# Kernel optimization log

Hardware: AMD Instinct MI355X
Metric: run time of the kernel (lower is better)

Reference implementation:

```python
import jax, jax.numpy as jnp
import numpy as np

E, D, MULT, K = 8, 1024, 4, 2   # num_experts, hidden_dim, mlp_multiplier, top-k
B, S = 4, 2048
H = MULT * D


def setup_inputs() -> dict:
    key = jax.random.key(0)
    k0, k1, k2, k3 = jax.random.split(key, 4)
    x = jax.random.normal(k0, (B, S, D), dtype=jnp.float32)
    Wr = jax.random.normal(k1, (E, D), dtype=jnp.float32) * (D ** -0.5)        # router (no bias)
    W1 = jax.random.normal(k2, (E, D, H), dtype=jnp.float32) * (D ** -0.5)     # expert fc1
    b1 = jnp.zeros((E, H), dtype=jnp.float32)
    W2 = jax.random.normal(k3, (E, H, D), dtype=jnp.float32) * (H ** -0.5)     # expert fc2
    b2 = jnp.zeros((E, D), dtype=jnp.float32)
    return {"x": x, "Wr": Wr, "W1": W1, "b1": b1, "W2": W2, "b2": b2}


def reference(x, Wr, W1, b1, W2, b2):
    # Router: softmax over experts then top-k -> per-token combine weights.
    probs = jax.nn.softmax(jnp.einsum("bsd,ed->bse", x, Wr), axis=-1)  # [B,S,E]
    topv, topi = jax.lax.top_k(probs, K)                                # [B,S,K]
    # combine[b,s,e] = sum_k topv * 1[topi==e]  (same math as the masked scatter-add)
    combine = jnp.sum(topv[..., None] * jax.nn.one_hot(topi, E, dtype=x.dtype), axis=2)  # [B,S,E]

    def body(acc, params):
        w1, bb1, w2, bb2, ce = params  # ce: [B,S] combine weight for this expert
        h = jax.nn.gelu(jnp.einsum("bsd,dh->bsh", x, w1) + bb1, approximate=False)
        y = jnp.einsum("bsh,hd->bsd", h, w2) + bb2
        return acc + ce[..., None] * y, None

    cE = jnp.moveaxis(combine, -1, 0)  # [E,B,S]
    out, _ = jax.lax.scan(body, jnp.zeros_like(x), (W1, b1, W2, b2, cE))
    return out
```

## Files before the change

kernel.cpp:

```cpp
#include <hip/hip_runtime.h>
#include <hip/hip_bf16.h>

#define E_   8
#define D_   1024
#define H_   4096
#define T_   8192
#define TMM  128
#define TNN  256
#define BK   64
#define CAP  17408
#define NBY  136
#define CK   2

typedef __attribute__((ext_vector_type(8))) short short8;
typedef __attribute__((ext_vector_type(4))) float floatx4;

__device__ __forceinline__ unsigned short f2bf(float f) {
    unsigned u = __float_as_uint(f);
    u += 0x7fffu + ((u >> 16) & 1u);
    return (unsigned short)(u >> 16);
}
__device__ __forceinline__ float bf2f(unsigned short u) {
    return __uint_as_float((unsigned)u << 16);
}

#define GLP16(g, l)                                                             \
    __builtin_amdgcn_global_load_lds((const __attribute__((address_space(1))) void*)(g), \
                                     (__attribute__((address_space(3))) void*)(l), 16, 0, 0)

__global__ __launch_bounds__(256) void router_kernel(
    const float* __restrict__ x, const float* __restrict__ Wr,
    int* __restrict__ cnt, int* __restrict__ tok_list,
    int2* __restrict__ inv_ei, float2* __restrict__ inv_w)
{
    int t = blockIdx.x * 4 + (threadIdx.x >> 6);
    int lane = threadIdx.x & 63;
    const float4* xr = (const float4*)(x + (size_t)t * D_);
    float acc[E_];
#pragma unroll
    for (int e = 0; e < E_; ++e) acc[e] = 0.f;
#pragma unroll
    for (int it = 0; it < D_ / 256; ++it) {
        float4 xv = xr[lane + it * 64];
#pragma unroll
        for (int e = 0; e < E_; ++e) {
            float4 wv = ((const float4*)(Wr + e * D_))[lane + it * 64];
            acc[e] += xv.x * wv.x + xv.y * wv.y + xv.z * wv.z + xv.w * wv.w;
        }
    }
#pragma unroll
    for (int e = 0; e < E_; ++e) {
#pragma unroll
        for (int off = 32; off; off >>= 1) acc[e] += __shfl_xor(acc[e], off);
    }
    if (lane == 0) {
        float m = acc[0];
#pragma unroll
        for (int e = 1; e < E_; ++e) m = fmaxf(m, acc[e]);
        float p[E_]; float s = 0.f;
#pragma unroll
        for (int e = 0; e < E_; ++e) { p[e] = expf(acc[e] - m); s += p[e]; }
        float inv = 1.f / s;
        int i1 = 0; float v1 = p[0];
#pragma unroll
        for (int e = 1; e < E_; ++e) if (p[e] > v1) { v1 = p[e]; i1 = e; }
        int i2 = -1; float v2 = -1.f;
#pragma unroll
        for (int e = 0; e < E_; ++e) { if (e == i1) continue; if (p[e] > v2) { v2 = p[e]; i2 = e; } }
        v1 *= inv; v2 *= inv;
        int pos1 = atomicAdd(&cnt[i1], 1);
        tok_list[i1 * T_ + pos1] = t;
        int pos2 = atomicAdd(&cnt[i2], 1);
        tok_list[i2 * T_ + pos2] = t;
        inv_ei[t] = make_int2(i1 | (pos1 << 3), i2 | (pos2 << 3));
        inv_w[t] = make_float2(v1, v2);
    }
}

__global__ void offsets_kernel(const int* __restrict__ cnt, int* __restrict__ start)
{
    if (threadIdx.x == 0) {
        int s = 0;
        for (int e = 0; e < E_; ++e) {
            start[e] = s;
            s += (cnt[e] + TMM - 1) / TMM * TMM;
        }
        start[E_] = s;
    }
}

__global__ __launch_bounds__(256) void gather_kernel(
    const float* __restrict__ x, const int* __restrict__ cnt, const int* __restrict__ start,
    const int* __restrict__ tok_list, unsigned short* __restrict__ xg)
{
    int row = blockIdx.x;
    int tid = threadIdx.x;
    int tot = start[E_];
    if (row >= tot) return;
    int e = 0;
    while (e < E_ - 1 && row >= start[e + 1]) ++e;
    int idx = row - start[e];
    unsigned short* dst = xg + (size_t)row * D_;
    if (idx < cnt[e]) {
        int t = tok_list[e * T_ + idx];
        const float4* src = (const float4*)(x + (size_t)t * D_);
        float4 v = src[tid];
        ushort4 o; o.x = f2bf(v.x); o.y = f2bf(v.y); o.z = f2bf(v.z); o.w = f2bf(v.w);
        ((ushort4*)dst)[tid] = o;
    } else {
        ((ushort4*)dst)[tid] = make_ushort4(0, 0, 0, 0);
    }
}

__global__ __launch_bounds__(256) void transpose_cvt(
    const float* __restrict__ W1, const float* __restrict__ W2,
    unsigned short* __restrict__ w1t, unsigned short* __restrict__ w2t)
{
    __shared__ float tile[64][65];
    int z = blockIdx.z;
    const float* src; unsigned short* dst; int R, C, r0, c0;
    if (z < 8) {
        src = W1 + (size_t)z * D_ * H_;       dst = w1t + (size_t)z * D_ * H_;
        R = D_; C = H_; r0 = blockIdx.y * 64; c0 = blockIdx.x * 64;
    } else {
        src = W2 + (size_t)(z - 8) * H_ * D_; dst = w2t + (size_t)(z - 8) * H_ * D_;
        R = H_; C = D_; r0 = blockIdx.x * 64; c0 = blockIdx.y * 64;
    }
    int t = threadIdx.x;
    int r = t >> 4, c4 = (t & 15) * 4;
#pragma unroll
    for (int p = 0; p < 4; ++p) {
        int row = p * 16 + r;
        float4 v = *(const float4*)(src + (size_t)(r0 + row) * C + c0 + c4);
        tile[row][c4 + 0] = v.x; tile[row][c4 + 1] = v.y;
        tile[row][c4 + 2] = v.z; tile[row][c4 + 3] = v.w;
    }
    __syncthreads();
#pragma unroll
    for (int p = 0; p < 4; ++p) {
        int orow = p * 16 + r;
        ushort4 o;
        o.x = f2bf(tile[c4 + 0][orow]); o.y = f2bf(tile[c4 + 1][orow]);
        o.z = f2bf(tile[c4 + 2][orow]); o.w = f2bf(tile[c4 + 3][orow]);
        *(ushort4*)(dst + (size_t)(c0 + orow) * R + r0 + c4) = o;
    }
}

__global__ __launch_bounds__(512) void fc1_kernel(
    const unsigned short* __restrict__ xg, const unsigned short* __restrict__ w1t,
    const float* __restrict__ b1, const int* __restrict__ start, unsigned short* __restrict__ h)
{
    __shared__ __align__(16) unsigned short Asm[TMM * BK];
    __shared__ __align__(16) unsigned short Bsm[TNN * BK];

    int row0 = blockIdx.y * TMM;
    int tot = start[E_];
    if (row0 >= tot) return;
    int e = 0;
    while (e < E_ - 1 && row0 >= start[e + 1]) ++e;

    int n0 = blockIdx.x * TNN;
    const unsigned short* Ag = xg + (size_t)row0 * D_;
    const unsigned short* Bg = w1t + (size_t)e * H_ * D_ + (size_t)n0 * D_;

    int tid = threadIdx.x;
    int wid = tid >> 6, lane = tid & 63;
    int wm = wid & 1, wn = wid >> 1;
    int quad = lane >> 4, r16 = lane & 15;
    int srow = lane >> 3;
    int scol = ((lane & 7) ^ srow) * 8;
    int rsw = r16 & 7;

    floatx4 acc[4][4];
#pragma unroll
    for (int i = 0; i < 4; ++i)
#pragma unroll
        for (int j = 0; j < 4; ++j) acc[i][j] = (floatx4){0.f, 0.f, 0.f, 0.f};

    for (int kc = 0; kc < D_ / BK; ++kc) {
        int k0 = kc * BK;
#pragma unroll
        for (int q = 0; q < 2; ++q) {
            int rb = wid * 16 + q * 8;
            GLP16(Ag + (size_t)(rb + srow) * D_ + k0 + scol, Asm + rb * BK);
        }
#pragma unroll
        for (int q = 0; q < 4; ++q) {
            int rb = wid * 32 + q * 8;
            GLP16(Bg + (size_t)(rb + srow) * D_ + k0 + scol, Bsm + rb * BK);
        }
        __syncthreads();
#pragma unroll
        for (int ks = 0; ks < 2; ++ks) {
            short8 af[4], bfr[4];
#pragma unroll
            for (int i = 0; i < 4; ++i)
                af[i] = *(const short8*)(Asm + (wm * 64 + i * 16 + r16) * BK + ((ks * 4 + quad) ^ rsw) * 8);
#pragma unroll
            for (int j = 0; j < 4; ++j)
                bfr[j] = *(const short8*)(Bsm + (wn * 64 + j * 16 + r16) * BK + ((ks * 4 + quad) ^ rsw) * 8);
#pragma unroll
            for (int i = 0; i < 4; ++i)
#pragma unroll
                for (int j = 0; j < 4; ++j)
                    acc[i][j] = __builtin_amdgcn_mfma_f32_16x16x32_bf16(af[i], bfr[j], acc[i][j], 0, 0, 0);
        }
        __syncthreads();
    }

    const float* b1e = b1 + (size_t)e * H_;
    float bj[4];
#pragma unroll
    for (int j = 0; j < 4; ++j) bj[j] = b1e[n0 + wn * 64 + j * 16 + r16];
#pragma unroll
    for (int i = 0; i < 4; ++i) {
#pragma unroll
        for (int r = 0; r < 4; ++r) {
            size_t rowg = (size_t)row0 + wm * 64 + i * 16 + quad * 4 + r;
            unsigned short* hp = h + rowg * H_ + n0 + wn * 64 + r16;
#pragma unroll
            for (int j = 0; j < 4; ++j) {
                float v = acc[i][j][r] + bj[j];
                float u = 1.5957691f * v * fmaf(0.044715f, v * v, 1.f);
                float gl = v * __builtin_amdgcn_rcpf(1.f + __expf(-u));
                hp[j * 16] = f2bf(gl);
            }
        }
    }
}

__global__ __launch_bounds__(512) void fc2_kernel(
    const unsigned short* __restrict__ h, const unsigned short* __restrict__ w2t,
    const int* __restrict__ start, unsigned short* __restrict__ y)
{
    __shared__ __align__(16) unsigned short Asm[TMM * BK];
    __shared__ __align__(16) unsigned short Bsm[TNN * BK];

    int row0 = blockIdx.y * TMM;
    int tot = start[E_];
    if (row0 >= tot) return;
    int e = 0;
    while (e < E_ - 1 && row0 >= start[e + 1]) ++e;

    int nblk = blockIdx.x & 3, ck = blockIdx.x >> 2;
    int n0 = nblk * TNN;
    const unsigned short* Ag = h + (size_t)row0 * H_;
    const unsigned short* Bg = w2t + (size_t)e * D_ * H_ + (size_t)n0 * H_;

    int tid = threadIdx.x;
    int wid = tid >> 6, lane = tid & 63;
    int wm = wid & 1, wn = wid >> 1;
    int quad = lane >> 4, r16 = lane & 15;
    int srow = lane >> 3;
    int scol = ((lane & 7) ^ srow) * 8;
    int rsw = r16 & 7;

    floatx4 acc[4][4];
#pragma unroll
    for (int i = 0; i < 4; ++i)
#pragma unroll
        for (int j = 0; j < 4; ++j) acc[i][j] = (floatx4){0.f, 0.f, 0.f, 0.f};

    const int KITERS = H_ / BK / CK;
    int kbase = ck * KITERS;
    for (int kc = kbase; kc < kbase + KITERS; ++kc) {
        int k0 = kc * BK;
#pragma unroll
        for (int q = 0; q < 2; ++q) {
            int rb = wid * 16 + q * 8;
            GLP16(Ag + (size_t)(rb + srow) * H_ + k0 + scol, Asm + rb * BK);
        }
#pragma unroll
        for (int q = 0; q < 4; ++q) {
            int rb = wid * 32 + q * 8;
            GLP16(Bg + (size_t)(rb + srow) * H_ + k0 + scol, Bsm + rb * BK);
        }
        __syncthreads();
#pragma unroll
        for (int ks = 0; ks < 2; ++ks) {
            short8 af[4], bfr[4];
#pragma unroll
            for (int i = 0; i < 4; ++i)
                af[i] = *(const short8*)(Asm + (wm * 64 + i * 16 + r16) * BK + ((ks * 4 + quad) ^ rsw) * 8);
#pragma unroll
            for (int j = 0; j < 4; ++j)
                bfr[j] = *(const short8*)(Bsm + (wn * 64 + j * 16 + r16) * BK + ((ks * 4 + quad) ^ rsw) * 8);
#pragma unroll
            for (int i = 0; i < 4; ++i)
#pragma unroll
                for (int j = 0; j < 4; ++j)
                    acc[i][j] = __builtin_amdgcn_mfma_f32_16x16x32_bf16(af[i], bfr[j], acc[i][j], 0, 0, 0);
        }
        __syncthreads();
    }

    unsigned short* ys = y + (size_t)ck * CAP * D_;
#pragma unroll
    for (int i = 0; i < 4; ++i) {
#pragma unroll
        for (int r = 0; r < 4; ++r) {
            int row = row0 + wm * 64 + i * 16 + quad * 4 + r;
            unsigned short* op = ys + (size_t)row * D_ + n0 + wn * 64 + r16;
#pragma unroll
            for (int j = 0; j < 4; ++j)
                op[j * 16] = f2bf(acc[i][j][r]);
        }
    }
}

__global__ __launch_bounds__(256) void combine_kernel(
    const unsigned short* __restrict__ y, const int* __restrict__ start,
    const int2* __restrict__ inv_ei, const float2* __restrict__ inv_w,
    const float* __restrict__ b2, float* __restrict__ out)
{
    int t = blockIdx.x;
    int tid = threadIdx.x;
    int2 ei = inv_ei[t];
    float2 w = inv_w[t];
    int e1 = ei.x & 7, x1 = ei.x >> 3;
    int e2 = ei.y & 7, x2 = ei.y >> 3;
    size_t r1 = (size_t)start[e1] + x1;
    size_t r2 = (size_t)start[e2] + x2;
    const size_t SL = (size_t)CAP * D_;
    ushort4 a0 = ((const ushort4*)(y + r1 * D_))[tid];
    ushort4 a1 = ((const ushort4*)(y + SL + r1 * D_))[tid];
    ushort4 c0 = ((const ushort4*)(y + r2 * D_))[tid];
    ushort4 c1 = ((const ushort4*)(y + SL + r2 * D_))[tid];
    float4 bA = ((const float4*)(b2 + (size_t)e1 * D_))[tid];
    float4 bB = ((const float4*)(b2 + (size_t)e2 * D_))[tid];
    float4 o;
    o.x = w.x * (bf2f(a0.x) + bf2f(a1.x) + bA.x) + w.y * (bf2f(c0.x) + bf2f(c1.x) + bB.x);
    o.y = w.x * (bf2f(a0.y) + bf2f(a1.y) + bA.y) + w.y * (bf2f(c0.y) + bf2f(c1.y) + bB.y);
    o.z = w.x * (bf2f(a0.z) + bf2f(a1.z) + bA.z) + w.y * (bf2f(c0.z) + bf2f(c1.z) + bB.z);
    o.w = w.x * (bf2f(a0.w) + bf2f(a1.w) + bA.w) + w.y * (bf2f(c0.w) + bf2f(c1.w) + bB.w);
    ((float4*)(out + (size_t)t * D_))[tid] = o;
}

extern "C" void kernel_launch(void* const* d_in, const int* in_sizes, int n_in,
                              void* d_out, int out_size, void* d_ws, size_t ws_size,
                              hipStream_t stream)
{
    const float* x  = (const float*)d_in[0];
    const float* Wr = (const float*)d_in[1];
    const float* W1 = (const float*)d_in[2];
    const float* b1 = (const float*)d_in[3];
    const float* W2 = (const float*)d_in[4];
    const float* b2 = (const float*)d_in[5];
    float* out = (float*)d_out;

    char* ws = (char*)d_ws;
    int*    cnt      = (int*)ws;
    int*    start    = (int*)(ws + 64);
    int*    tok_list = (int*)(ws + 256);
    int2*   inv_ei   = (int2*)(ws + 393216);
    float2* inv_w    = (float2*)(ws + 458752);
    char* p0 = ws + (1u << 20);
    unsigned short* xg  = (unsigned short*)p0;
    unsigned short* w1t = (unsigned short*)(p0 + 35651584ull);
    unsigned short* h   = (unsigned short*)(p0 + 35651584ull + 67108864ull);
    unsigned short* w2t = (unsigned short*)(p0 + 35651584ull + 67108864ull + 142606336ull);
    unsigned short* y   = (unsigned short*)p0;
    (void)ws_size; (void)in_sizes; (void)n_in; (void)out_size;

    hipMemsetAsync(ws, 0, 64, stream);

    transpose_cvt<<<dim3(64, 16, 16), 256, 0, stream>>>(W1, W2, w1t, w2t);
    router_kernel<<<T_ / 4, 256, 0, stream>>>(x, Wr, cnt, tok_list, inv_ei, inv_w);
    offsets_kernel<<<1, 64, 0, stream>>>(cnt, start);
    gather_kernel<<<CAP, 256, 0, stream>>>(x, cnt, start, tok_list, xg);
    fc1_kernel<<<dim3(H_ / TNN, NBY), 512, 0, stream>>>(xg, w1t, b1, start, h);
    fc2_kernel<<<dim3((D_ / TNN) * CK, NBY), 512, 0, stream>>>(h, w2t, start, y);
    combine_kernel<<<T_, 256, 0, stream>>>(y, start, inv_ei, inv_w, b2, out);
}
```

Before: 914.5 us.

## Fuse fp32 weight transpose and bf16 conversion into GEMM B-tile loads

Removes the separate transpose_cvt pass that wrote bf16 transposed copies of W1 and W2. The fc1 and fc2 kernels now read fp32 weights directly with float4 loads, convert them to bf16 in registers and scatter them transposed into swizzled shared memory. This saves a full read/write pass over both weight tensors each call. In exchange, every M-tile block re-reads fp32 weights (twice the bytes of bf16) through synchronous register loads instead of async global-to-LDS copies, and the launch bounds now request 4 blocks per CU.

```diff
diff --git a/kernel.cpp b/kernel.cpp
--- a/kernel.cpp
+++ b/kernel.cpp
@@ -112,42 +112,8 @@
     }
 }
 
-__global__ __launch_bounds__(256) void transpose_cvt(
-    const float* __restrict__ W1, const float* __restrict__ W2,
-    unsigned short* __restrict__ w1t, unsigned short* __restrict__ w2t)
-{
-    __shared__ float tile[64][65];
-    int z = blockIdx.z;
-    const float* src; unsigned short* dst; int R, C, r0, c0;
-    if (z < 8) {
-        src = W1 + (size_t)z * D_ * H_;       dst = w1t + (size_t)z * D_ * H_;
-        R = D_; C = H_; r0 = blockIdx.y * 64; c0 = blockIdx.x * 64;
-    } else {
-        src = W2 + (size_t)(z - 8) * H_ * D_; dst = w2t + (size_t)(z - 8) * H_ * D_;
-        R = H_; C = D_; r0 = blockIdx.x * 64; c0 = blockIdx.y * 64;
-    }
-    int t = threadIdx.x;
-    int r = t >> 4, c4 = (t & 15) * 4;
-#pragma unroll
-    for (int p = 0; p < 4; ++p) {
-        int row = p * 16 + r;
-        float4 v = *(const float4*)(src + (size_t)(r0 + row) * C + c0 + c4);
-        tile[row][c4 + 0] = v.x; tile[row][c4 + 1] = v.y;
-        tile[row][c4 + 2] = v.z; tile[row][c4 + 3] = v.w;
-    }
-    __syncthreads();
-#pragma unroll
-    for (int p = 0; p < 4; ++p) {
-        int orow = p * 16 + r;
-        ushort4 o;
-        o.x = f2bf(tile[c4 + 0][orow]); o.y = f2bf(tile[c4 + 1][orow]);
-        o.z = f2bf(tile[c4 + 2][orow]); o.w = f2bf(tile[c4 + 3][orow]);
-        *(ushort4*)(dst + (size_t)(c0 + orow) * R + r0 + c4) = o;
-    }
-}
-
-__global__ __launch_bounds__(512) void fc1_kernel(
-    const unsigned short* __restrict__ xg, const unsigned short* __restrict__ w1t,
+__global__ __launch_bounds__(512, 4) void fc1_kernel(
+    const unsigned short* __restrict__ xg, const float* __restrict__ W1,
     const float* __restrict__ b1, const int* __restrict__ start, unsigned short* __restrict__ h)
 {
     __shared__ __align__(16) unsigned short Asm[TMM * BK];
@@ -161,7 +127,7 @@
 
     int n0 = blockIdx.x * TNN;
     const unsigned short* Ag = xg + (size_t)row0 * D_;
-    const unsigned short* Bg = w1t + (size_t)e * H_ * D_ + (size_t)n0 * D_;
+    const float* Bg = W1 + (size_t)e * D_ * H_ + n0;
 
     int tid = threadIdx.x;
     int wid = tid >> 6, lane = tid & 63;
@@ -170,6 +136,8 @@
     int srow = lane >> 3;
     int scol = ((lane & 7) ^ srow) * 8;
     int rsw = r16 & 7;
+    int gsl = (wid + (lane >> 4)) & 7;
+    int kparl = (lane >> 3) & 1;
 
     floatx4 acc[4][4];
 #pragma unroll
@@ -185,9 +153,19 @@
             GLP16(Ag + (size_t)(rb + srow) * D_ + k0 + scol, Asm + rb * BK);
         }
 #pragma unroll
-        for (int q = 0; q < 4; ++q) {
-            int rb = wid * 32 + q * 8;
-            GLP16(Bg + (size_t)(rb + srow) * D_ + k0 + scol, Bsm + rb * BK);
+        for (int m = 0; m < 2; ++m) {
+            int k4 = gsl * 2 + (kparl ^ m);
+            const float* src = Bg + (size_t)(k0 + k4 * 4) * H_ + 4 * lane;
+            float4 r0 = *(const float4*)(src);
+            float4 r1 = *(const float4*)(src + H_);
+            float4 r2 = *(const float4*)(src + 2 * H_);
+            float4 r3 = *(const float4*)(src + 3 * H_);
+            int h2 = (k4 & 1) * 4;
+#define BW_(J, c) { int nrow = 4 * lane + J;                                         \
+        ushort4 o; o.x = f2bf(r0.c); o.y = f2bf(r1.c); o.z = f2bf(r2.c); o.w = f2bf(r3.c); \
+        *(ushort4*)(Bsm + nrow * BK + ((gsl ^ (nrow & 7)) << 3) + h2) = o; }
+            BW_(0, x) BW_(1, y) BW_(2, z) BW_(3, w)
+#undef BW_
         }
         __syncthreads();
 #pragma unroll
@@ -229,8 +207,8 @@
     }
 }
 
-__global__ __launch_bounds__(512) void fc2_kernel(
-    const unsigned short* __restrict__ h, const unsigned short* __restrict__ w2t,
+__global__ __launch_bounds__(512, 4) void fc2_kernel(
+    const unsigned short* __restrict__ h, const float* __restrict__ W2,
     const int* __restrict__ start, unsigned short* __restrict__ y)
 {
     __shared__ __align__(16) unsigned short Asm[TMM * BK];
@@ -245,7 +223,7 @@
     int nblk = blockIdx.x & 3, ck = blockIdx.x >> 2;
     int n0 = nblk * TNN;
     const unsigned short* Ag = h + (size_t)row0 * H_;
-    const unsigned short* Bg = w2t + (size_t)e * D_ * H_ + (size_t)n0 * H_;
+    const float* Bg = W2 + (size_t)e * H_ * D_ + n0;
 
     int tid = threadIdx.x;
     int wid = tid >> 6, lane = tid & 63;
@@ -254,6 +232,8 @@
     int srow = lane >> 3;
     int scol = ((lane & 7) ^ srow) * 8;
     int rsw = r16 & 7;
+    int gsl = (wid + (lane >> 4)) & 7;
+    int kparl = (lane >> 3) & 1;
 
     floatx4 acc[4][4];
 #pragma unroll
@@ -271,9 +251,19 @@
             GLP16(Ag + (size_t)(rb + srow) * H_ + k0 + scol, Asm + rb * BK);
         }
 #pragma unroll
-        for (int q = 0; q < 4; ++q) {
-            int rb = wid * 32 + q * 8;
-            GLP16(Bg + (size_t)(rb + srow) * H_ + k0 + scol, Bsm + rb * BK);
+        for (int m = 0; m < 2; ++m) {
+            int k4 = gsl * 2 + (kparl ^ m);
+            const float* src = Bg + (size_t)(k0 + k4 * 4) * D_ + 4 * lane;
+            float4 r0 = *(const float4*)(src);
+            float4 r1 = *(const float4*)(src + D_);
+            float4 r2 = *(const float4*)(src + 2 * D_);
+            float4 r3 = *(const float4*)(src + 3 * D_);
+            int h2 = (k4 & 1) * 4;
+#define BW_(J, c) { int nrow = 4 * lane + J;                                         \
+        ushort4 o; o.x = f2bf(r0.c); o.y = f2bf(r1.c); o.z = f2bf(r2.c); o.w = f2bf(r3.c); \
+        *(ushort4*)(Bsm + nrow * BK + ((gsl ^ (nrow & 7)) << 3) + h2) = o; }
+            BW_(0, x) BW_(1, y) BW_(2, z) BW_(3, w)
+#undef BW_
         }
         __syncthreads();
 #pragma unroll
@@ -355,20 +345,17 @@
     int2*   inv_ei   = (int2*)(ws + 393216);
     float2* inv_w    = (float2*)(ws + 458752);
     char* p0 = ws + (1u << 20);
-    unsigned short* xg  = (unsigned short*)p0;
-    unsigned short* w1t = (unsigned short*)(p0 + 35651584ull);
-    unsigned short* h   = (unsigned short*)(p0 + 35651584ull + 67108864ull);
-    unsigned short* w2t = (unsigned short*)(p0 + 35651584ull + 67108864ull + 142606336ull);
-    unsigned short* y   = (unsigned short*)p0;
+    unsigned short* xg = (unsigned short*)p0;
+    unsigned short* h  = (unsigned short*)(p0 + 35651584ull);
+    unsigned short* y  = (unsigned short*)(p0 + 35651584ull + 142606336ull);
     (void)ws_size; (void)in_sizes; (void)n_in; (void)out_size;
 
     hipMemsetAsync(ws, 0, 64, stream);
 
-    transpose_cvt<<<dim3(64, 16, 16), 256, 0, stream>>>(W1, W2, w1t, w2t);
     router_kernel<<<T_ / 4, 256, 0, stream>>>(x, Wr, cnt, tok_list, inv_ei, inv_w);
     offsets_kernel<<<1, 64, 0, stream>>>(cnt, start);
     gather_kernel<<<CAP, 256, 0, stream>>>(x, cnt, start, tok_list, xg);
-    fc1_kernel<<<dim3(H_ / TNN, NBY), 512, 0, stream>>>(xg, w1t, b1, start, h);
-    fc2_kernel<<<dim3((D_ / TNN) * CK, NBY), 512, 0, stream>>>(h, w2t, start, y);
+    fc1_kernel<<<dim3(H_ / TNN, NBY), 512, 0, stream>>>(xg, W1, b1, start, h);
+    fc2_kernel<<<dim3((D_ / TNN) * CK, NBY), 512, 0, stream>>>(h, W2, start, y);
     combine_kernel<<<T_, 256, 0, stream>>>(y, start, inv_ei, inv_w, b2, out);
 }
```

Measured after the change: 1.039 ms. 13.6% more time.
